# Performance work log

Measured on AMD Instinct MI355X. Metric: run time of the kernel, lower is better.

The kernel has to match this reference:

```python
import jax, jax.numpy as jnp
import numpy as np

N_NODES = 50000
N_EDGES = 800000
IN_DIM = 128
HID = 64
HEADS = 4
OUT = 16
N_GRAPHS = 500
NEG_SLOPE = 0.2


def setup_inputs() -> dict:
    key = jax.random.key(0)
    ks = jax.random.split(key, 12)
    x = jax.random.normal(ks[0], (N_NODES, IN_DIM), dtype=jnp.float32)
    edge_index = jax.random.randint(ks[1], (2, N_EDGES), 0, N_NODES, dtype=jnp.int64)
    batch = jnp.sort(jax.random.randint(ks[2], (N_NODES,), 0, N_GRAPHS, dtype=jnp.int64))
    s1 = 1.0 / np.sqrt(IN_DIM)
    s2 = 1.0 / np.sqrt(HID)
    W1 = jax.random.normal(ks[3], (IN_DIM, HEADS * HID), dtype=jnp.float32) * s1
    a1_src = jax.random.normal(ks[4], (HEADS, HID), dtype=jnp.float32) * s2
    a1_dst = jax.random.normal(ks[5], (HEADS, HID), dtype=jnp.float32) * s2
    b1 = jnp.zeros((HID,), dtype=jnp.float32)
    W2 = jax.random.normal(ks[6], (HID, HEADS * HID), dtype=jnp.float32) * s2
    a2_src = jax.random.normal(ks[7], (HEADS, HID), dtype=jnp.float32) * s2
    a2_dst = jax.random.normal(ks[8], (HEADS, HID), dtype=jnp.float32) * s2
    b2 = jnp.zeros((HID,), dtype=jnp.float32)
    fcW = jax.random.normal(ks[9], (HID, OUT), dtype=jnp.float32) * s2
    fcb = jnp.zeros((OUT,), dtype=jnp.float32)
    return {"x": x, "edge_index": edge_index, "batch": batch,
            "W1": W1, "a1_src": a1_src, "a1_dst": a1_dst, "b1": b1,
            "W2": W2, "a2_src": a2_src, "a2_dst": a2_dst, "b2": b2,
            "fcW": fcW, "fcb": fcb}


def gat_conv(x, W, a_src, a_dst, b, src, dst):
    # PyG GATConv with concat=False: per-head linear, edge softmax over dst, head-mean.
    n = x.shape[0]
    h = (x @ W).reshape(n, HEADS, HID)          # [N,H,D]
    alpha_s = jnp.sum(h * a_src, axis=-1)        # [N,H]
    alpha_d = jnp.sum(h * a_dst, axis=-1)        # [N,H]
    e = jax.nn.leaky_relu(alpha_s[src] + alpha_d[dst], NEG_SLOPE)  # [E,H]
    emax = jax.ops.segment_max(e, dst, num_segments=n)
    ex = jnp.exp(e - emax[dst])
    denom = jax.ops.segment_sum(ex, dst, num_segments=n)
    alpha = ex / denom[dst]                      # [E,H], edge softmax per dst
    msg = h[src] * alpha[:, :, None]             # [E,H,D]
    out = jax.ops.segment_sum(msg, dst, num_segments=n)  # [N,H,D]
    return out.mean(axis=1) + b                  # concat=False -> head mean


def reference(x, edge_index, batch, W1, a1_src, a1_dst, b1, W2, a2_src, a2_dst, b2, fcW, fcb):
    n = x.shape[0]
    # PyG GATConv default add_self_loops=True
    loops = jnp.arange(n, dtype=edge_index.dtype)
    src = jnp.concatenate([edge_index[0], loops])
    dst = jnp.concatenate([edge_index[1], loops])
    h = jax.nn.relu(gat_conv(x, W1, a1_src, a1_dst, b1, src, dst))
    h = jax.nn.relu(gat_conv(h, W2, a2_src, a2_dst, b2, src, dst))
    # global_mean_pool over batch ids
    sums = jax.ops.segment_sum(h, batch, num_segments=N_GRAPHS)
    counts = jax.ops.segment_sum(jnp.ones((n,), dtype=h.dtype), batch, num_segments=N_GRAPHS)
    pooled = sums / jnp.clip(counts, 1.0)[:, None]
    return pooled @ fcW + fcb
```

## Files before the change

kernel.cpp:

```cpp
#include <hip/hip_runtime.h>
#include <hip/hip_bf16.h>
#include <hip/hip_fp16.h>

#define NN 50000
#define EE 800000
#define ETOT 850000
#define NG 500
#define NBLK ((NN + 255) / 256)

typedef __attribute__((ext_vector_type(8))) short bf16x8;
typedef __attribute__((ext_vector_type(4))) float f32x4;

__device__ __forceinline__ unsigned short bf16_rne(float v) {
    unsigned u = __float_as_uint(v);
    unsigned r = u + 0x7FFFu + ((u >> 16) & 1u);
    return (unsigned short)(r >> 16);
}

__global__ void k_detect(const int* __restrict__ ei, int* __restrict__ flag) {
    unsigned long long b = __ballot(ei[2 * threadIdx.x + 1] != 0);
    if (threadIdx.x == 0) *flag = b ? 1 : 2;
}

__global__ __launch_bounds__(256) void k_prep(const int* __restrict__ ei,
                                              const int* __restrict__ flag,
                                              int* __restrict__ src32,
                                              int* __restrict__ dst32,
                                              int* __restrict__ deg) {
    int e = blockIdx.x * 256 + threadIdx.x;
    if (e >= ETOT) return;
    int st = *flag;
    int s, d;
    if (e < EE) {
        s = ei[(size_t)st * e];
        d = ei[(size_t)st * (EE + e)];
    } else {
        s = d = e - EE;
    }
    src32[e] = s;
    dst32[e] = d;
    atomicAdd(&deg[d], 1);
}

__global__ __launch_bounds__(256) void k_blocksum(const int* __restrict__ deg,
                                                  int* __restrict__ bsum) {
    __shared__ int l[256];
    int gid = blockIdx.x * 256 + threadIdx.x;
    int tid = threadIdx.x;
    l[tid] = (gid < NN) ? deg[gid] : 0;
    __syncthreads();
    for (int o = 128; o > 0; o >>= 1) {
        if (tid < o) l[tid] += l[tid + o];
        __syncthreads();
    }
    if (tid == 0) bsum[blockIdx.x] = l[0];
}

__global__ __launch_bounds__(256) void k_scan_bsum(const int* __restrict__ bsum,
                                                   int* __restrict__ boff) {
    __shared__ int l[256];
    int tid = threadIdx.x;
    int v = (tid < NBLK) ? bsum[tid] : 0;
    l[tid] = v;
    __syncthreads();
    for (int d = 1; d < 256; d <<= 1) {
        int t = (tid >= d) ? l[tid - d] : 0;
        __syncthreads();
        l[tid] += t;
        __syncthreads();
    }
    if (tid < NBLK) boff[tid] = l[tid] - v;
}

__global__ __launch_bounds__(256) void k_scan_final(const int* __restrict__ deg,
                                                    const int* __restrict__ boff,
                                                    int* __restrict__ rowptr,
                                                    int* __restrict__ cursor) {
    __shared__ int l[256];
    int gid = blockIdx.x * 256 + threadIdx.x;
    int tid = threadIdx.x;
    int v = (gid < NN) ? deg[gid] : 0;
    l[tid] = v;
    __syncthreads();
    for (int d = 1; d < 256; d <<= 1) {
        int t = (tid >= d) ? l[tid - d] : 0;
        __syncthreads();
        l[tid] += t;
        __syncthreads();
    }
    int ex = l[tid] - v + boff[blockIdx.x];
    if (gid < NN) { rowptr[gid] = ex; cursor[gid] = ex; }
    if (gid == 0) rowptr[NN] = ETOT;
}

__global__ __launch_bounds__(256) void k_scatter(const int* __restrict__ src32,
                                                 const int* __restrict__ dst32,
                                                 int* __restrict__ cursor,
                                                 int* __restrict__ csr_src) {
    int e = blockIdx.x * 256 + threadIdx.x;
    if (e >= ETOT) return;
    int pos = atomicAdd(&cursor[dst32[e]], 1);
    csr_src[pos] = src32[e];
}

template <int K>
__global__ __launch_bounds__(256) void k_prepw(const float* __restrict__ W,
                                               const float* __restrict__ asrc,
                                               const float* __restrict__ adst,
                                               unsigned short* __restrict__ bhi,
                                               unsigned short* __restrict__ blo,
                                               float* __restrict__ aperm,
                                               float* __restrict__ adperm) {
    int t = blockIdx.x * 256 + threadIdx.x;
    int j = t / K, k = t - j * K;
    int d = j >> 2, h = j & 3;
    float v = W[k * 256 + h * 64 + d];
    unsigned short hb = bf16_rne(v);
    float hf = __uint_as_float((unsigned)hb << 16);
    bhi[t] = hb;
    blo[t] = bf16_rne(v - hf);
    if (k == 0) { aperm[j] = asrc[h * 64 + d]; adperm[j] = adst[h * 64 + d]; }
}

template <int K>
__global__ __launch_bounds__(256) void k_gemm_mfma(
        const float* __restrict__ A,
        const unsigned short* __restrict__ Bhi,
        const unsigned short* __restrict__ Blo,
        const float* __restrict__ aperm,
        const float* __restrict__ adperm,
        __half* __restrict__ C16,
        float* __restrict__ os,
        float* __restrict__ od, int M) {
    const int NC = K / 32;
    int wave = threadIdx.x >> 6;
    int lane = threadIdx.x & 63;
    int l = lane & 15, q = lane >> 4;
    int m0 = blockIdx.x * 64 + wave * 16;
    if (m0 >= M) return;

    bf16x8 ahi[NC], alo[NC];
    const float* arow = A + (size_t)(m0 + l) * K + q * 8;
#pragma unroll
    for (int c = 0; c < NC; ++c) {
        float4 v0 = *(const float4*)(arow + c * 32);
        float4 v1 = *(const float4*)(arow + c * 32 + 4);
        float vv[8] = {v0.x, v0.y, v0.z, v0.w, v1.x, v1.y, v1.z, v1.w};
#pragma unroll
        for (int j = 0; j < 8; ++j) {
            unsigned short hb = bf16_rne(vv[j]);
            float hf = __uint_as_float((unsigned)hb << 16);
            ahi[c][j] = (short)hb;
            alo[c][j] = (short)bf16_rne(vv[j] - hf);
        }
    }

    float ps[4] = {0.f, 0.f, 0.f, 0.f}, pd[4] = {0.f, 0.f, 0.f, 0.f};
    const size_t brow = (size_t)l * K + q * 8;
#pragma unroll 2
    for (int n = 0; n < 16; ++n) {
        f32x4 acc = {0.f, 0.f, 0.f, 0.f};
        const unsigned short* bh = Bhi + (size_t)(n * 16) * K + brow;
        const unsigned short* bl = Blo + (size_t)(n * 16) * K + brow;
#pragma unroll
        for (int c = 0; c < NC; ++c) {
            bf16x8 bhf = *(const bf16x8*)(bh + c * 32);
            bf16x8 blf = *(const bf16x8*)(bl + c * 32);
            acc = __builtin_amdgcn_mfma_f32_16x16x32_bf16(ahi[c], bhf, acc, 0, 0, 0);
            acc = __builtin_amdgcn_mfma_f32_16x16x32_bf16(ahi[c], blf, acc, 0, 0, 0);
            acc = __builtin_amdgcn_mfma_f32_16x16x32_bf16(alo[c], bhf, acc, 0, 0, 0);
        }
        float av = aperm[n * 16 + l], dv = adperm[n * 16 + l];
#pragma unroll
        for (int r = 0; r < 4; ++r) {
            ps[r] += acc[r] * av;
            pd[r] += acc[r] * dv;
            C16[(size_t)(m0 + q * 4 + r) * 256 + n * 16 + l] = __float2half(acc[r]);
        }
    }
#pragma unroll
    for (int r = 0; r < 4; ++r) {
        ps[r] += __shfl_xor(ps[r], 4);
        ps[r] += __shfl_xor(ps[r], 8);
        pd[r] += __shfl_xor(pd[r], 4);
        pd[r] += __shfl_xor(pd[r], 8);
    }
    if (l < 4) {
#pragma unroll
        for (int r = 0; r < 4; ++r) {
            os[(size_t)(m0 + q * 4 + r) * 4 + l] = ps[r];
            od[(size_t)(m0 + q * 4 + r) * 4 + l] = pd[r];
        }
    }
}

__device__ __forceinline__ float lrelu_exp(float x) {
    x = x > 0.f ? x : 0.2f * x;
    return __expf(x);
}

__global__ __launch_bounds__(256) void k_aggr(const int* __restrict__ rowptr,
                                              const int* __restrict__ csr_src,
                                              const float* __restrict__ as_,
                                              const float* __restrict__ ad_,
                                              const __half* __restrict__ h16,
                                              const float* __restrict__ bias,
                                              float* __restrict__ out) {
    int d = (blockIdx.x * 256 + threadIdx.x) >> 6;
    int lane = threadIdx.x & 63;
    if (d >= NN) return;
    int beg = rowptr[d], end = rowptr[d + 1];
    float4 adv = *(const float4*)(ad_ + d * 4);

    int s0 = 0;
    float4 u0 = make_float4(0.f, 0.f, 0.f, 0.f);
    float4 den = make_float4(0.f, 0.f, 0.f, 0.f);
    int i0 = beg + lane;
    if (i0 < end) {
        s0 = csr_src[i0];
        float4 sv = *(const float4*)(as_ + s0 * 4);
        u0.x = lrelu_exp(sv.x + adv.x);
        u0.y = lrelu_exp(sv.y + adv.y);
        u0.z = lrelu_exp(sv.z + adv.z);
        u0.w = lrelu_exp(sv.w + adv.w);
        den = u0;
    }
    for (int i = i0 + 64; i < end; i += 64) {
        int s = csr_src[i];
        float4 sv = *(const float4*)(as_ + s * 4);
        den.x += lrelu_exp(sv.x + adv.x);
        den.y += lrelu_exp(sv.y + adv.y);
        den.z += lrelu_exp(sv.z + adv.z);
        den.w += lrelu_exp(sv.w + adv.w);
    }
#pragma unroll
    for (int off = 32; off > 0; off >>= 1) {
        den.x += __shfl_xor(den.x, off);
        den.y += __shfl_xor(den.y, off);
        den.z += __shfl_xor(den.z, off);
        den.w += __shfl_xor(den.w, off);
    }
    float4 dinv = make_float4(0.25f / den.x, 0.25f / den.y,
                              0.25f / den.z, 0.25f / den.w);

    float4 al0 = make_float4(u0.x * dinv.x, u0.y * dinv.y,
                             u0.z * dinv.z, u0.w * dinv.w);
    int cnt = end - beg;
    if (cnt > 64) cnt = 64;
    int cnt4 = (cnt + 3) & ~3;
    float acc = 0.f;
    uint2 r0, r1, r2, r3;
    {
        int sa = __shfl(s0, 0), sb = __shfl(s0, 1);
        int sc = __shfl(s0, 2), sd = __shfl(s0, 3);
        r0 = *(const uint2*)(h16 + (size_t)sa * 256 + lane * 4);
        r1 = *(const uint2*)(h16 + (size_t)sb * 256 + lane * 4);
        r2 = *(const uint2*)(h16 + (size_t)sc * 256 + lane * 4);
        r3 = *(const uint2*)(h16 + (size_t)sd * 256 + lane * 4);
    }
    for (int j = 0; j < cnt4; j += 4) {
        int sa = __shfl(s0, (j + 4) & 63), sb = __shfl(s0, (j + 5) & 63);
        int sc = __shfl(s0, (j + 6) & 63), sd = __shfl(s0, (j + 7) & 63);
        uint2 n0 = *(const uint2*)(h16 + (size_t)sa * 256 + lane * 4);
        uint2 n1 = *(const uint2*)(h16 + (size_t)sb * 256 + lane * 4);
        uint2 n2 = *(const uint2*)(h16 + (size_t)sc * 256 + lane * 4);
        uint2 n3 = *(const uint2*)(h16 + (size_t)sd * 256 + lane * 4);
        float a00 = __shfl(al0.x, j),     a01 = __shfl(al0.y, j),     a02 = __shfl(al0.z, j),     a03 = __shfl(al0.w, j);
        float a10 = __shfl(al0.x, j + 1), a11 = __shfl(al0.y, j + 1), a12 = __shfl(al0.z, j + 1), a13 = __shfl(al0.w, j + 1);
        float a20 = __shfl(al0.x, j + 2), a21 = __shfl(al0.y, j + 2), a22 = __shfl(al0.z, j + 2), a23 = __shfl(al0.w, j + 2);
        float a30 = __shfl(al0.x, j + 3), a31 = __shfl(al0.y, j + 3), a32 = __shfl(al0.z, j + 3), a33 = __shfl(al0.w, j + 3);
        float2 fa, fb;
        fa = __half22float2(*(const __half2*)&r0.x);
        fb = __half22float2(*(const __half2*)&r0.y);
        acc += a00 * fa.x + a01 * fa.y + a02 * fb.x + a03 * fb.y;
        fa = __half22float2(*(const __half2*)&r1.x);
        fb = __half22float2(*(const __half2*)&r1.y);
        acc += a10 * fa.x + a11 * fa.y + a12 * fb.x + a13 * fb.y;
        fa = __half22float2(*(const __half2*)&r2.x);
        fb = __half22float2(*(const __half2*)&r2.y);
        acc += a20 * fa.x + a21 * fa.y + a22 * fb.x + a23 * fb.y;
        fa = __half22float2(*(const __half2*)&r3.x);
        fb = __half22float2(*(const __half2*)&r3.y);
        acc += a30 * fa.x + a31 * fa.y + a32 * fb.x + a33 * fb.y;
        r0 = n0; r1 = n1; r2 = n2; r3 = n3;
    }
    for (int chunk = beg + 64; chunk < end; chunk += 64) {
        int i = chunk + lane;
        int s = 0;
        float4 al = make_float4(0.f, 0.f, 0.f, 0.f);
        if (i < end) {
            s = csr_src[i];
            float4 sv = *(const float4*)(as_ + s * 4);
            al.x = lrelu_exp(sv.x + adv.x) * dinv.x;
            al.y = lrelu_exp(sv.y + adv.y) * dinv.y;
            al.z = lrelu_exp(sv.z + adv.z) * dinv.z;
            al.w = lrelu_exp(sv.w + adv.w) * dinv.w;
        }
        int cc = end - chunk;
        if (cc > 64) cc = 64;
        for (int j = 0; j < cc; ++j) {
            int sj = __shfl(s, j);
            float a0 = __shfl(al.x, j), a1 = __shfl(al.y, j);
            float a2 = __shfl(al.z, j), a3 = __shfl(al.w, j);
            uint2 raw = *(const uint2*)(h16 + (size_t)sj * 256 + lane * 4);
            float2 fa = __half22float2(*(const __half2*)&raw.x);
            float2 fb = __half22float2(*(const __half2*)&raw.y);
            acc += a0 * fa.x + a1 * fa.y + a2 * fb.x + a3 * fb.y;
        }
    }
    float v = acc + bias[lane];
    out[d * 64 + lane] = v > 0.f ? v : 0.f;
}

__global__ __launch_bounds__(256) void k_pool_fc(const float* __restrict__ x3,
                                                 const int* __restrict__ batch,
                                                 const int* __restrict__ flag,
                                                 const float* __restrict__ fcW,
                                                 const float* __restrict__ fcb,
                                                 float* __restrict__ out) {
    int g = blockIdx.x;
    int tid = threadIdx.x, lane = tid & 63, w = tid >> 6;
    int st = *flag;
    int lo = 0, hi = NN;
    while (lo < hi) { int mid = (lo + hi) >> 1; if (batch[(size_t)st * mid] < g) lo = mid + 1; else hi = mid; }
    int start = lo;
    hi = NN;
    while (lo < hi) { int mid = (lo + hi) >> 1; if (batch[(size_t)st * mid] < g + 1) lo = mid + 1; else hi = mid; }
    int end = lo;
    float sum = 0.f;
    for (int n = start + w; n < end; n += 4) sum += x3[n * 64 + lane];
    __shared__ float ls[4][64];
    ls[w][lane] = sum;
    __syncthreads();
    if (w == 0) {
        float c = (float)(end - start);
        if (c < 1.f) c = 1.f;
        float p = (ls[0][lane] + ls[1][lane] + ls[2][lane] + ls[3][lane]) / c;
#pragma unroll
        for (int o = 0; o < 16; ++o) {
            float v = p * fcW[lane * 16 + o];
#pragma unroll
            for (int off = 32; off > 0; off >>= 1) v += __shfl_down(v, off);
            if (lane == 0) out[g * 16 + o] = v + fcb[o];
        }
    }
}

extern "C" void kernel_launch(void* const* d_in, const int* in_sizes, int n_in,
                              void* d_out, int out_size, void* d_ws, size_t ws_size,
                              hipStream_t stream) {
    const float* x   = (const float*)d_in[0];
    const int*   ei  = (const int*)d_in[1];
    const int*   bat = (const int*)d_in[2];
    const float* W1  = (const float*)d_in[3];
    const float* a1s = (const float*)d_in[4];
    const float* a1d = (const float*)d_in[5];
    const float* b1  = (const float*)d_in[6];
    const float* W2  = (const float*)d_in[7];
    const float* a2s = (const float*)d_in[8];
    const float* a2d = (const float*)d_in[9];
    const float* b2  = (const float*)d_in[10];
    const float* fcW = (const float*)d_in[11];
    const float* fcb = (const float*)d_in[12];
    float* out = (float*)d_out;

    float* ws = (float*)d_ws;
    int* flag = (int*)d_ws;
    __half* h16  = (__half*)(ws + 256);
    float* as_   = (float*)(h16 + (size_t)NN * 256);
    float* ad_   = as_ + NN * 4;
    float* xacc  = ad_ + NN * 4;
    int* src32   = (int*)(xacc + (size_t)NN * 64);
    int* dst32   = src32 + ETOT;
    int* deg     = dst32 + ETOT;
    int* rowptr  = deg + NN;
    int* cursor  = rowptr + NN + 1;
    int* csr_src = cursor + NN;
    int* bsum    = csr_src + ETOT;
    int* boff    = bsum + NBLK;
    char* p = (char*)(boff + NBLK);
    p = (char*)(((size_t)p + 255) & ~(size_t)255);
    unsigned short* bt1h = (unsigned short*)p; p += 256 * 128 * 2;
    unsigned short* bt1l = (unsigned short*)p; p += 256 * 128 * 2;
    unsigned short* bt2h = (unsigned short*)p; p += 256 * 64 * 2;
    unsigned short* bt2l = (unsigned short*)p; p += 256 * 64 * 2;
    float* ap1  = (float*)p; p += 256 * 4;
    float* adp1 = (float*)p; p += 256 * 4;
    float* ap2  = (float*)p; p += 256 * 4;
    float* adp2 = (float*)p; p += 256 * 4;

    const int eb = (ETOT + 255) / 256;
    const int wb = (NN * 64 + 255) / 256;

    k_detect<<<1, 64, 0, stream>>>(ei, flag);
    hipMemsetAsync(deg, 0, NN * sizeof(int), stream);
    k_prep<<<eb, 256, 0, stream>>>(ei, flag, src32, dst32, deg);
    k_prepw<128><<<128, 256, 0, stream>>>(W1, a1s, a1d, bt1h, bt1l, ap1, adp1);
    k_prepw<64><<<64, 256, 0, stream>>>(W2, a2s, a2d, bt2h, bt2l, ap2, adp2);
    k_blocksum<<<NBLK, 256, 0, stream>>>(deg, bsum);
    k_scan_bsum<<<1, 256, 0, stream>>>(bsum, boff);
    k_scan_final<<<NBLK, 256, 0, stream>>>(deg, boff, rowptr, cursor);
    k_scatter<<<eb, 256, 0, stream>>>(src32, dst32, cursor, csr_src);

    const int gg = (NN + 63) / 64;
    k_gemm_mfma<128><<<gg, 256, 0, stream>>>(x, bt1h, bt1l, ap1, adp1, h16, as_, ad_, NN);
    k_aggr<<<wb, 256, 0, stream>>>(rowptr, csr_src, as_, ad_, h16, b1, xacc);
    k_gemm_mfma<64><<<gg, 256, 0, stream>>>(xacc, bt2h, bt2l, ap2, adp2, h16, as_, ad_, NN);
    k_aggr<<<wb, 256, 0, stream>>>(rowptr, csr_src, as_, ad_, h16, b2, xacc);
    k_pool_fc<<<NG, 256, 0, stream>>>(xacc, bat, flag, fcW, fcb, out);
}
```

Measured before the change: 444.7 us.

## Register-block GEMM over two row tiles, stage aggr indices in LDS, merge prep kernels

The GEMM now runs one wave per block and computes two 16-row tiles, so each loaded B fragment feeds two MFMA chains. Row indices are clamped, with guarded stores for the tail. The aggregation kernel stages attention weights and source indices in shared memory and reads them as vectors, replacing many per-edge shuffles. The stride-detection kernel is inlined into its consumers and the two weight-prep kernels are merged, removing launches at the cost of redundant detection work in every block.

```diff
diff --git a/kernel.cpp b/kernel.cpp
--- a/kernel.cpp
+++ b/kernel.cpp
@@ -17,19 +17,25 @@
     return (unsigned short)(r >> 16);
 }
 
-__global__ void k_detect(const int* __restrict__ ei, int* __restrict__ flag) {
-    unsigned long long b = __ballot(ei[2 * threadIdx.x + 1] != 0);
-    if (threadIdx.x == 0) *flag = b ? 1 : 2;
+__device__ __forceinline__ int detect_stride(const int* __restrict__ ei,
+                                             int tid, int* sflag) {
+    if (tid < 64) {
+        unsigned long long b = __ballot(ei[2 * tid + 1] != 0);
+        if (tid == 0) *sflag = b ? 1 : 2;
+    }
+    __syncthreads();
+    return *sflag;
 }
 
 __global__ __launch_bounds__(256) void k_prep(const int* __restrict__ ei,
-                                              const int* __restrict__ flag,
                                               int* __restrict__ src32,
                                               int* __restrict__ dst32,
                                               int* __restrict__ deg) {
-    int e = blockIdx.x * 256 + threadIdx.x;
+    __shared__ int sflag;
+    int tid = threadIdx.x;
+    int st = detect_stride(ei, tid, &sflag);
+    int e = blockIdx.x * 256 + tid;
     if (e >= ETOT) return;
-    int st = *flag;
     int s, d;
     if (e < EE) {
         s = ei[(size_t)st * e];
@@ -103,15 +109,14 @@
     csr_src[pos] = src32[e];
 }
 
-template <int K>
-__global__ __launch_bounds__(256) void k_prepw(const float* __restrict__ W,
-                                               const float* __restrict__ asrc,
-                                               const float* __restrict__ adst,
-                                               unsigned short* __restrict__ bhi,
-                                               unsigned short* __restrict__ blo,
-                                               float* __restrict__ aperm,
-                                               float* __restrict__ adperm) {
-    int t = blockIdx.x * 256 + threadIdx.x;
+__device__ __forceinline__ void prepw_one(const float* __restrict__ W,
+                                          const float* __restrict__ asrc,
+                                          const float* __restrict__ adst,
+                                          unsigned short* __restrict__ bhi,
+                                          unsigned short* __restrict__ blo,
+                                          float* __restrict__ ap,
+                                          float* __restrict__ adp,
+                                          int K, int t) {
     int j = t / K, k = t - j * K;
     int d = j >> 2, h = j & 3;
     float v = W[k * 256 + h * 64 + d];
@@ -119,11 +124,27 @@
     float hf = __uint_as_float((unsigned)hb << 16);
     bhi[t] = hb;
     blo[t] = bf16_rne(v - hf);
-    if (k == 0) { aperm[j] = asrc[h * 64 + d]; adperm[j] = adst[h * 64 + d]; }
+    if (k == 0) { ap[j] = asrc[h * 64 + d]; adp[j] = adst[h * 64 + d]; }
+}
+
+__global__ __launch_bounds__(256) void k_prepw(
+        const float* __restrict__ W1, const float* __restrict__ a1s,
+        const float* __restrict__ a1d, const float* __restrict__ W2,
+        const float* __restrict__ a2s, const float* __restrict__ a2d,
+        unsigned short* __restrict__ b1h, unsigned short* __restrict__ b1l,
+        unsigned short* __restrict__ b2h, unsigned short* __restrict__ b2l,
+        float* __restrict__ ap1, float* __restrict__ adp1,
+        float* __restrict__ ap2, float* __restrict__ adp2) {
+    int g = blockIdx.x;
+    if (g < 128) {
+        prepw_one(W1, a1s, a1d, b1h, b1l, ap1, adp1, 128, g * 256 + threadIdx.x);
+    } else {
+        prepw_one(W2, a2s, a2d, b2h, b2l, ap2, adp2, 64, (g - 128) * 256 + threadIdx.x);
+    }
 }
 
 template <int K>
-__global__ __launch_bounds__(256) void k_gemm_mfma(
+__global__ __launch_bounds__(64) void k_gemm_mfma(
         const float* __restrict__ A,
         const unsigned short* __restrict__ Bhi,
         const unsigned short* __restrict__ Blo,
@@ -133,64 +154,84 @@
         float* __restrict__ os,
         float* __restrict__ od, int M) {
     const int NC = K / 32;
-    int wave = threadIdx.x >> 6;
-    int lane = threadIdx.x & 63;
+    int lane = threadIdx.x;
     int l = lane & 15, q = lane >> 4;
-    int m0 = blockIdx.x * 64 + wave * 16;
-    if (m0 >= M) return;
-
-    bf16x8 ahi[NC], alo[NC];
-    const float* arow = A + (size_t)(m0 + l) * K + q * 8;
-#pragma unroll
-    for (int c = 0; c < NC; ++c) {
-        float4 v0 = *(const float4*)(arow + c * 32);
-        float4 v1 = *(const float4*)(arow + c * 32 + 4);
-        float vv[8] = {v0.x, v0.y, v0.z, v0.w, v1.x, v1.y, v1.z, v1.w};
-#pragma unroll
-        for (int j = 0; j < 8; ++j) {
-            unsigned short hb = bf16_rne(vv[j]);
-            float hf = __uint_as_float((unsigned)hb << 16);
-            ahi[c][j] = (short)hb;
-            alo[c][j] = (short)bf16_rne(vv[j] - hf);
-        }
-    }
-
-    float ps[4] = {0.f, 0.f, 0.f, 0.f}, pd[4] = {0.f, 0.f, 0.f, 0.f};
+    int m0 = blockIdx.x * 32;
+
+    bf16x8 ahi[2][NC], alo[2][NC];
+#pragma unroll
+    for (int t = 0; t < 2; ++t) {
+        int row = m0 + t * 16 + l;
+        if (row >= M) row = M - 1;
+        const float* arow = A + (size_t)row * K + q * 8;
+#pragma unroll
+        for (int c = 0; c < NC; ++c) {
+            float4 v0 = *(const float4*)(arow + c * 32);
+            float4 v1 = *(const float4*)(arow + c * 32 + 4);
+            float vv[8] = {v0.x, v0.y, v0.z, v0.w, v1.x, v1.y, v1.z, v1.w};
+#pragma unroll
+            for (int j = 0; j < 8; ++j) {
+                unsigned short hb = bf16_rne(vv[j]);
+                float hf = __uint_as_float((unsigned)hb << 16);
+                ahi[t][c][j] = (short)hb;
+                alo[t][c][j] = (short)bf16_rne(vv[j] - hf);
+            }
+        }
+    }
+
+    float ps[2][4] = {}, pd[2][4] = {};
     const size_t brow = (size_t)l * K + q * 8;
 #pragma unroll 2
     for (int n = 0; n < 16; ++n) {
-        f32x4 acc = {0.f, 0.f, 0.f, 0.f};
         const unsigned short* bh = Bhi + (size_t)(n * 16) * K + brow;
         const unsigned short* bl = Blo + (size_t)(n * 16) * K + brow;
+        bf16x8 bhf[NC], blf[NC];
 #pragma unroll
         for (int c = 0; c < NC; ++c) {
-            bf16x8 bhf = *(const bf16x8*)(bh + c * 32);
-            bf16x8 blf = *(const bf16x8*)(bl + c * 32);
-            acc = __builtin_amdgcn_mfma_f32_16x16x32_bf16(ahi[c], bhf, acc, 0, 0, 0);
-            acc = __builtin_amdgcn_mfma_f32_16x16x32_bf16(ahi[c], blf, acc, 0, 0, 0);
-            acc = __builtin_amdgcn_mfma_f32_16x16x32_bf16(alo[c], bhf, acc, 0, 0, 0);
+            bhf[c] = *(const bf16x8*)(bh + c * 32);
+            blf[c] = *(const bf16x8*)(bl + c * 32);
+        }
+        f32x4 acc0 = {0.f, 0.f, 0.f, 0.f}, acc1 = {0.f, 0.f, 0.f, 0.f};
+#pragma unroll
+        for (int c = 0; c < NC; ++c) {
+            acc0 = __builtin_amdgcn_mfma_f32_16x16x32_bf16(ahi[0][c], bhf[c], acc0, 0, 0, 0);
+            acc1 = __builtin_amdgcn_mfma_f32_16x16x32_bf16(ahi[1][c], bhf[c], acc1, 0, 0, 0);
+            acc0 = __builtin_amdgcn_mfma_f32_16x16x32_bf16(ahi[0][c], blf[c], acc0, 0, 0, 0);
+            acc1 = __builtin_amdgcn_mfma_f32_16x16x32_bf16(ahi[1][c], blf[c], acc1, 0, 0, 0);
+            acc0 = __builtin_amdgcn_mfma_f32_16x16x32_bf16(alo[0][c], bhf[c], acc0, 0, 0, 0);
+            acc1 = __builtin_amdgcn_mfma_f32_16x16x32_bf16(alo[1][c], bhf[c], acc1, 0, 0, 0);
         }
         float av = aperm[n * 16 + l], dv = adperm[n * 16 + l];
 #pragma unroll
         for (int r = 0; r < 4; ++r) {
-            ps[r] += acc[r] * av;
-            pd[r] += acc[r] * dv;
-            C16[(size_t)(m0 + q * 4 + r) * 256 + n * 16 + l] = __float2half(acc[r]);
-        }
-    }
-#pragma unroll
-    for (int r = 0; r < 4; ++r) {
-        ps[r] += __shfl_xor(ps[r], 4);
-        ps[r] += __shfl_xor(ps[r], 8);
-        pd[r] += __shfl_xor(pd[r], 4);
-        pd[r] += __shfl_xor(pd[r], 8);
-    }
+            ps[0][r] += acc0[r] * av; pd[0][r] += acc0[r] * dv;
+            ps[1][r] += acc1[r] * av; pd[1][r] += acc1[r] * dv;
+            int gm0 = m0 + q * 4 + r;
+            if (gm0 < M) C16[(size_t)gm0 * 256 + n * 16 + l] = __float2half(acc0[r]);
+            int gm1 = m0 + 16 + q * 4 + r;
+            if (gm1 < M) C16[(size_t)gm1 * 256 + n * 16 + l] = __float2half(acc1[r]);
+        }
+    }
+#pragma unroll
+    for (int t = 0; t < 2; ++t)
+#pragma unroll
+        for (int r = 0; r < 4; ++r) {
+            ps[t][r] += __shfl_xor(ps[t][r], 4);
+            ps[t][r] += __shfl_xor(ps[t][r], 8);
+            pd[t][r] += __shfl_xor(pd[t][r], 4);
+            pd[t][r] += __shfl_xor(pd[t][r], 8);
+        }
     if (l < 4) {
 #pragma unroll
-        for (int r = 0; r < 4; ++r) {
-            os[(size_t)(m0 + q * 4 + r) * 4 + l] = ps[r];
-            od[(size_t)(m0 + q * 4 + r) * 4 + l] = pd[r];
-        }
+        for (int t = 0; t < 2; ++t)
+#pragma unroll
+            for (int r = 0; r < 4; ++r) {
+                int gm = m0 + t * 16 + q * 4 + r;
+                if (gm < M) {
+                    os[(size_t)gm * 4 + l] = ps[t][r];
+                    od[(size_t)gm * 4 + l] = pd[t][r];
+                }
+            }
     }
 }
 
@@ -206,8 +247,11 @@
                                               const __half* __restrict__ h16,
                                               const float* __restrict__ bias,
                                               float* __restrict__ out) {
-    int d = (blockIdx.x * 256 + threadIdx.x) >> 6;
+    __shared__ float als[4][256];
+    __shared__ int sss[4][64];
+    int w = threadIdx.x >> 6;
     int lane = threadIdx.x & 63;
+    int d = blockIdx.x * 4 + w;
     if (d >= NN) return;
     int beg = rowptr[d], end = rowptr[d + 1];
     float4 adv = *(const float4*)(ad_ + d * 4);
@@ -242,46 +286,44 @@
     }
     float4 dinv = make_float4(0.25f / den.x, 0.25f / den.y,
                               0.25f / den.z, 0.25f / den.w);
-
     float4 al0 = make_float4(u0.x * dinv.x, u0.y * dinv.y,
                              u0.z * dinv.z, u0.w * dinv.w);
+    *(float4*)&als[w][lane * 4] = al0;
+    sss[w][lane] = s0;
+
     int cnt = end - beg;
     if (cnt > 64) cnt = 64;
     int cnt4 = (cnt + 3) & ~3;
     float acc = 0.f;
-    uint2 r0, r1, r2, r3;
-    {
-        int sa = __shfl(s0, 0), sb = __shfl(s0, 1);
-        int sc = __shfl(s0, 2), sd = __shfl(s0, 3);
-        r0 = *(const uint2*)(h16 + (size_t)sa * 256 + lane * 4);
-        r1 = *(const uint2*)(h16 + (size_t)sb * 256 + lane * 4);
-        r2 = *(const uint2*)(h16 + (size_t)sc * 256 + lane * 4);
-        r3 = *(const uint2*)(h16 + (size_t)sd * 256 + lane * 4);
-    }
+    int4 sq = *(const int4*)&sss[w][0];
+    uint2 r0 = *(const uint2*)(h16 + (size_t)sq.x * 256 + lane * 4);
+    uint2 r1 = *(const uint2*)(h16 + (size_t)sq.y * 256 + lane * 4);
+    uint2 r2 = *(const uint2*)(h16 + (size_t)sq.z * 256 + lane * 4);
+    uint2 r3 = *(const uint2*)(h16 + (size_t)sq.w * 256 + lane * 4);
     for (int j = 0; j < cnt4; j += 4) {
-        int sa = __shfl(s0, (j + 4) & 63), sb = __shfl(s0, (j + 5) & 63);
-        int sc = __shfl(s0, (j + 6) & 63), sd = __shfl(s0, (j + 7) & 63);
-        uint2 n0 = *(const uint2*)(h16 + (size_t)sa * 256 + lane * 4);
-        uint2 n1 = *(const uint2*)(h16 + (size_t)sb * 256 + lane * 4);
-        uint2 n2 = *(const uint2*)(h16 + (size_t)sc * 256 + lane * 4);
-        uint2 n3 = *(const uint2*)(h16 + (size_t)sd * 256 + lane * 4);
-        float a00 = __shfl(al0.x, j),     a01 = __shfl(al0.y, j),     a02 = __shfl(al0.z, j),     a03 = __shfl(al0.w, j);
-        float a10 = __shfl(al0.x, j + 1), a11 = __shfl(al0.y, j + 1), a12 = __shfl(al0.z, j + 1), a13 = __shfl(al0.w, j + 1);
-        float a20 = __shfl(al0.x, j + 2), a21 = __shfl(al0.y, j + 2), a22 = __shfl(al0.z, j + 2), a23 = __shfl(al0.w, j + 2);
-        float a30 = __shfl(al0.x, j + 3), a31 = __shfl(al0.y, j + 3), a32 = __shfl(al0.z, j + 3), a33 = __shfl(al0.w, j + 3);
+        int jn = (j + 4) & 63;
+        int4 sn = *(const int4*)&sss[w][jn];
+        uint2 n0 = *(const uint2*)(h16 + (size_t)sn.x * 256 + lane * 4);
+        uint2 n1 = *(const uint2*)(h16 + (size_t)sn.y * 256 + lane * 4);
+        uint2 n2 = *(const uint2*)(h16 + (size_t)sn.z * 256 + lane * 4);
+        uint2 n3 = *(const uint2*)(h16 + (size_t)sn.w * 256 + lane * 4);
+        float4 a0 = *(const float4*)&als[w][j * 4];
+        float4 a1 = *(const float4*)&als[w][j * 4 + 4];
+        float4 a2 = *(const float4*)&als[w][j * 4 + 8];
+        float4 a3 = *(const float4*)&als[w][j * 4 + 12];
         float2 fa, fb;
         fa = __half22float2(*(const __half2*)&r0.x);
         fb = __half22float2(*(const __half2*)&r0.y);
-        acc += a00 * fa.x + a01 * fa.y + a02 * fb.x + a03 * fb.y;
+        acc += a0.x * fa.x + a0.y * fa.y + a0.z * fb.x + a0.w * fb.y;
         fa = __half22float2(*(const __half2*)&r1.x);
         fb = __half22float2(*(const __half2*)&r1.y);
-        acc += a10 * fa.x + a11 * fa.y + a12 * fb.x + a13 * fb.y;
+        acc += a1.x * fa.x + a1.y * fa.y + a1.z * fb.x + a1.w * fb.y;
         fa = __half22float2(*(const __half2*)&r2.x);
         fb = __half22float2(*(const __half2*)&r2.y);
-        acc += a20 * fa.x + a21 * fa.y + a22 * fb.x + a23 * fb.y;
+        acc += a2.x * fa.x + a2.y * fa.y + a2.z * fb.x + a2.w * fb.y;
         fa = __half22float2(*(const __half2*)&r3.x);
         fb = __half22float2(*(const __half2*)&r3.y);
-        acc += a30 * fa.x + a31 * fa.y + a32 * fb.x + a33 * fb.y;
+        acc += a3.x * fa.x + a3.y * fa.y + a3.z * fb.x + a3.w * fb.y;
         r0 = n0; r1 = n1; r2 = n2; r3 = n3;
     }
     for (int chunk = beg + 64; chunk < end; chunk += 64) {
@@ -314,13 +356,14 @@
 
 __global__ __launch_bounds__(256) void k_pool_fc(const float* __restrict__ x3,
                                                  const int* __restrict__ batch,
-                                                 const int* __restrict__ flag,
+                                                 const int* __restrict__ ei,
                                                  const float* __restrict__ fcW,
                                                  const float* __restrict__ fcb,
                                                  float* __restrict__ out) {
+    __shared__ int sflag;
+    int tid = threadIdx.x, lane = tid & 63, w = tid >> 6;
+    int st = detect_stride(ei, tid, &sflag);
     int g = blockIdx.x;
-    int tid = threadIdx.x, lane = tid & 63, w = tid >> 6;
-    int st = *flag;
     int lo = 0, hi = NN;
     while (lo < hi) { int mid = (lo + hi) >> 1; if (batch[(size_t)st * mid] < g) lo = mid + 1; else hi = mid; }
     int start = lo;
@@ -365,7 +408,6 @@
     float* out = (float*)d_out;
 
     float* ws = (float*)d_ws;
-    int* flag = (int*)d_ws;
     __half* h16  = (__half*)(ws + 256);
     float* as_   = (float*)(h16 + (size_t)NN * 256);
     float* ad_   = as_ + NN * 4;
@@ -392,20 +434,20 @@
     const int eb = (ETOT + 255) / 256;
     const int wb = (NN * 64 + 255) / 256;
 
-    k_detect<<<1, 64, 0, stream>>>(ei, flag);
     hipMemsetAsync(deg, 0, NN * sizeof(int), stream);
-    k_prep<<<eb, 256, 0, stream>>>(ei, flag, src32, dst32, deg);
-    k_prepw<128><<<128, 256, 0, stream>>>(W1, a1s, a1d, bt1h, bt1l, ap1, adp1);
-    k_prepw<64><<<64, 256, 0, stream>>>(W2, a2s, a2d, bt2h, bt2l, ap2, adp2);
+    k_prep<<<eb, 256, 0, stream>>>(ei, src32, dst32, deg);
+    k_prepw<<<192, 256, 0, stream>>>(W1, a1s, a1d, W2, a2s, a2d,
+                                     bt1h, bt1l, bt2h, bt2l,
+                                     ap1, adp1, ap2, adp2);
     k_blocksum<<<NBLK, 256, 0, stream>>>(deg, bsum);
     k_scan_bsum<<<1, 256, 0, stream>>>(bsum, boff);
     k_scan_final<<<NBLK, 256, 0, stream>>>(deg, boff, rowptr, cursor);
     k_scatter<<<eb, 256, 0, stream>>>(src32, dst32, cursor, csr_src);
 
-    const int gg = (NN + 63) / 64;
-    k_gemm_mfma<128><<<gg, 256, 0, stream>>>(x, bt1h, bt1l, ap1, adp1, h16, as_, ad_, NN);
+    const int gg = (NN + 31) / 32;
+    k_gemm_mfma<128><<<gg, 64, 0, stream>>>(x, bt1h, bt1l, ap1, adp1, h16, as_, ad_, NN);
     k_aggr<<<wb, 256, 0, stream>>>(rowptr, csr_src, as_, ad_, h16, b1, xacc);
-    k_gemm_mfma<64><<<gg, 256, 0, stream>>>(xacc, bt2h, bt2l, ap2, adp2, h16, as_, ad_, NN);
+    k_gemm_mfma<64><<<gg, 64, 0, stream>>>(xacc, bt2h, bt2l, ap2, adp2, h16, as_, ad_, NN);
     k_aggr<<<wb, 256, 0, stream>>>(rowptr, csr_src, as_, ad_, h16, b2, xacc);
-    k_pool_fc<<<NG, 256, 0, stream>>>(xacc, bat, flag, fcW, fcb, out);
-}
+    k_pool_fc<<<NG, 256, 0, stream>>>(xacc, bat, ei, fcW, fcb, out);
+}
```

Measured after the change: 379.1 us. 1.17x faster.
